# Kernel optimization log

Measured on AMD Instinct MI355X. Metric: run time of the kernel, lower is better.

Reference implementation:

```python
import jax, jax.numpy as jnp
import numpy as np

NEG_SLOPE = 0.2  # PyG GATConv default negative_slope
H, C = 4, 64     # heads, per-head channels


def gat_layer(x, src, dst, edge_attr, W, a_src, a_dst, We, a_e, b):
    """PyG-style GATConv with edge features, concat=True. src/dst include self loops."""
    N = x.shape[0]
    h = (x @ W).reshape(N, H, C)                      # [N,H,C]
    al_s = (h * a_src[None]).sum(-1)                  # [N,H]
    al_d = (h * a_dst[None]).sum(-1)                  # [N,H]
    eh = (edge_attr @ We).reshape(-1, H, C)           # [E,H,C]
    al_e = (eh * a_e[None]).sum(-1)                   # [E,H]
    alpha = jax.nn.leaky_relu(al_s[src] + al_d[dst] + al_e, NEG_SLOPE)  # [E,H]
    # softmax over incoming edges of each destination node
    m = jax.ops.segment_max(alpha, dst, num_segments=N)
    p = jnp.exp(alpha - m[dst])
    denom = jax.ops.segment_sum(p, dst, num_segments=N)
    w = p / (denom[dst] + 1e-16)                      # [E,H]
    msg = h[src] * w[..., None]                       # [E,H,C]
    out = jax.ops.segment_sum(msg, dst, num_segments=N)  # [N,H,C]
    return out.reshape(N, H * C) + b


def setup_inputs() -> dict:
    key = jax.random.key(0)
    ks = jax.random.split(key, 20)
    N, E = 50000, 800000
    s = 0.05
    inp = {
        'x': jax.random.normal(ks[0], (N, 5), jnp.float32),
        'edge_index': jax.random.randint(ks[1], (2, E), 0, N, jnp.int32),
        'edge_attr': jax.random.normal(ks[2], (E, 4), jnp.float32),
        'W0': jax.random.normal(ks[3], (5, 256), jnp.float32) * s,
        'a_src0': jax.random.normal(ks[4], (H, C), jnp.float32) * s,
        'a_dst0': jax.random.normal(ks[5], (H, C), jnp.float32) * s,
        'We0': jax.random.normal(ks[6], (4, 256), jnp.float32) * s,
        'a_e0': jax.random.normal(ks[7], (H, C), jnp.float32) * s,
        'b0': jnp.zeros((256,), jnp.float32),
        'W1': jax.random.normal(ks[8], (256, 256), jnp.float32) * s,
        'a_src1': jax.random.normal(ks[9], (H, C), jnp.float32) * s,
        'a_dst1': jax.random.normal(ks[10], (H, C), jnp.float32) * s,
        'We1': jax.random.normal(ks[11], (4, 256), jnp.float32) * s,
        'a_e1': jax.random.normal(ks[12], (H, C), jnp.float32) * s,
        'b1': jnp.zeros((256,), jnp.float32),
        'Wm1': jax.random.normal(ks[13], (768, 128), jnp.float32) * s,
        'bm1': jnp.zeros((128,), jnp.float32),
        'Wm2': jax.random.normal(ks[14], (128, 64), jnp.float32) * s,
        'bm2': jnp.zeros((64,), jnp.float32),
        'Wm3': jax.random.normal(ks[15], (64, 128), jnp.float32) * s,
        'bm3': jnp.zeros((128,), jnp.float32),
    }
    return inp


def reference(x, edge_index, edge_attr,
              W0, a_src0, a_dst0, We0, a_e0, b0,
              W1, a_src1, a_dst1, We1, a_e1, b1,
              Wm1, bm1, Wm2, bm2, Wm3, bm3):
    N = x.shape[0]
    # add self loops once; self-loop edge_attr = mean of edge_attr (PyG fill_value='mean')
    loops = jnp.arange(N, dtype=edge_index.dtype)
    src = jnp.concatenate([edge_index[0], loops])
    dst = jnp.concatenate([edge_index[1], loops])
    mean_ea = jnp.mean(edge_attr, axis=0, keepdims=True)
    ea = jnp.concatenate([edge_attr, jnp.broadcast_to(mean_ea, (N, edge_attr.shape[1]))], axis=0)

    h = gat_layer(x, src, dst, ea, W0, a_src0, a_dst0, We0, a_e0, b0)
    h = jax.nn.relu(h)  # dropout is identity in eval
    h = gat_layer(h, src, dst, ea, W1, a_src1, a_dst1, We1, a_e1, b1)

    mean_pool = jnp.mean(h, axis=0)                      # [256]
    max_pool = jnp.max(h, axis=0)                        # [256]
    att = jax.nn.softmax(jnp.sum(h * mean_pool[None], axis=1))  # [N]
    att_pool = jnp.sum(h * att[:, None], axis=0)         # [256]
    comb = jnp.concatenate([mean_pool, max_pool, att_pool])  # [768]

    z = jax.nn.relu(comb @ Wm1 + bm1)
    z = jax.nn.relu(z @ Wm2 + bm2)
    g = z @ Wm3 + bm3
    return g[None]  # [1,128]
```

## Files before the change

### kernel.cpp

```cpp
#include <hip/hip_runtime.h>
#include <hip/hip_fp16.h>
#include <type_traits>

static const long long N_ = 50000;
static const long long E_ = 800000;
static const int NCOPY = 8;
#define LOG2E 1.44269504088896f

typedef __attribute__((ext_vector_type(8))) short bf16x8;
typedef __attribute__((ext_vector_type(4))) float f32x4;

__device__ __forceinline__ float lrelu(float x){ return x >= 0.f ? x : 0.2f*x; }
__device__ __forceinline__ unsigned fkey(float x){
  unsigned u = __float_as_uint(x);
  return (u & 0x80000000u) ? ~u : (u | 0x80000000u);
}
__device__ __forceinline__ float unfkey(unsigned k){
  return __uint_as_float((k & 0x80000000u) ? (k & 0x7fffffffu) : ~k);
}
__device__ __forceinline__ unsigned h2u(__half2 h){ return *(unsigned*)&h; }

__global__ void k_pre(const int* __restrict__ ei, int* __restrict__ deg8,
                      unsigned char* __restrict__ rank,
                      const float* __restrict__ W1, ushort* __restrict__ Bhi,
                      ushort* __restrict__ Blo){
  int t = threadIdx.x;
  long long e = (long long)blockIdx.x*256 + t;
  if (e < E_){
    int d = ei[E_ + e];
    int copy = blockIdx.x & (NCOPY-1);
    int old = atomicAdd(&deg8[copy*(int)N_ + d], 1);
    rank[e] = (unsigned char)old;
  }
  if (blockIdx.x < 256){
    int k = blockIdx.x, n = t;
    float v = W1[k*256+n];
    unsigned u = __float_as_uint(v);
    ushort hi = (ushort)(u>>16);
    float rem = v - __uint_as_float(u & 0xffff0000u);
    unsigned ur = __float_as_uint(rem);
    ushort lo = (ushort)((ur + 0x7fff + ((ur>>16)&1)) >> 16);
    int tl = n>>4, kb = k>>5, q = (k>>3)&3, j = k&7;
    long long idx = ((((long long)tl*8+kb)*64 + q*16 + (n&15))<<3) + j;
    Bhi[idx] = hi; Blo[idx] = lo;
  }
}

__global__ void k_scan1(const int* __restrict__ deg8, int* __restrict__ bsum,
                        const float* __restrict__ ea, float* __restrict__ eapart){
  __shared__ int lds[256];
  __shared__ float fl[256];
  int t = threadIdx.x;
  long long idx = (long long)blockIdx.x*256 + t;
  int v = 0;
  if (idx < N_){
    #pragma unroll
    for (int c=0;c<NCOPY;c++) v += deg8[c*(int)N_ + idx];
  }
  lds[t] = v;
  float s = 0.f;
  for (long long i = (long long)blockIdx.x*256 + t; i < E_*4; i += (long long)gridDim.x*256)
    s += ea[i];
  fl[t] = s;
  __syncthreads();
  for (int st=128; st>=1; st>>=1){
    if (t<st) lds[t] += lds[t+st];
    if (t<st && st>=4) fl[t] += fl[t+st];
    __syncthreads();
  }
  if (t==0) bsum[blockIdx.x] = lds[0];
  if (t<4) eapart[blockIdx.x*4 + t] = fl[t];
}

__global__ void k_scan2(const int* __restrict__ bsum, int* __restrict__ bpre, int nb,
                        int* __restrict__ rowptr,
                        const float* __restrict__ We0, const float* __restrict__ ae0,
                        const float* __restrict__ We1, const float* __restrict__ ae1,
                        const float* __restrict__ eapart, float* __restrict__ small){
  __shared__ int lds[256];
  __shared__ float sea[4];
  int t = threadIdx.x;
  int v = (t < nb) ? bsum[t] : 0;
  lds[t] = v; __syncthreads();
  for (int off=1; off<256; off<<=1){
    int add = (t>=off) ? lds[t-off] : 0;
    __syncthreads();
    lds[t] += add;
    __syncthreads();
  }
  if (t < nb) bpre[t] = lds[t] - v;
  if (t == 0) rowptr[N_] = (int)E_;
  if (t < 4){
    float s = 0.f;
    for (int b=0;b<nb;b++) s += eapart[b*4+t];
    sea[t] = s;
  }
  if (t < 32){
    int l = t>>4, f = (t>>2)&3, h = t&3;
    const float* We = l ? We1 : We0;
    const float* ae = l ? ae1 : ae0;
    float s = 0.f;
    for (int cc=0; cc<64; cc++) s += We[f*256 + h*64 + cc]*ae[h*64+cc];
    small[l*16 + f*4 + h] = s * LOG2E;
  }
  __syncthreads();
  if (t < 8){
    int l = t>>2, h = t&3;
    const float* Ae = small + l*16;
    const float invE = 1.f/(float)E_;
    float s = 0.f;
    for (int f=0; f<4; f++) s += sea[f]*invE*Ae[f*4+h];
    small[32 + l*4 + h] = s;
  }
}

__global__ void k_scan3(const int* __restrict__ deg8, const int* __restrict__ bpre,
                        int* __restrict__ rowptr, int* __restrict__ base){
  __shared__ int lds[256];
  int t = threadIdx.x;
  long long idx = (long long)blockIdx.x*256 + t;
  int dd[NCOPY]; int v = 0;
  if (idx < N_){
    #pragma unroll
    for (int c=0;c<NCOPY;c++){ dd[c] = deg8[c*(int)N_ + idx]; v += dd[c]; }
  }
  lds[t] = v; __syncthreads();
  for (int off=1; off<256; off<<=1){
    int add = (t>=off) ? lds[t-off] : 0;
    __syncthreads();
    lds[t] += add;
    __syncthreads();
  }
  if (idx < N_){
    int rp = bpre[blockIdx.x] + lds[t] - v;
    rowptr[idx] = rp;
    int cum = rp;
    #pragma unroll
    for (int c=0;c<NCOPY;c++){ base[c*(int)N_ + idx] = cum; cum += dd[c]; }
  }
}

__global__ void k_h0(const float* __restrict__ x, const float* __restrict__ W0,
                     const float* __restrict__ as0, const float* __restrict__ ad0,
                     __half* __restrict__ h0, float* __restrict__ als, float* __restrict__ ald){
  int wid = (int)(((long long)blockIdx.x*blockDim.x + threadIdx.x) >> 6);
  int lane = threadIdx.x & 63;
  if (wid >= (int)N_) return;
  const float* xr = x + wid*5;
  float xv[5];
  #pragma unroll
  for (int f=0; f<5; f++) xv[f] = xr[f];
  int c = lane*4;
  float a0=0,a1=0,a2=0,a3=0;
  #pragma unroll
  for (int f=0; f<5; f++){
    const float* wr = W0 + f*256 + c;
    a0 += xv[f]*wr[0]; a1 += xv[f]*wr[1]; a2 += xv[f]*wr[2]; a3 += xv[f]*wr[3];
  }
  uint2 pk = make_uint2(h2u(__floats2half2_rn(a0,a1)), h2u(__floats2half2_rn(a2,a3)));
  *(uint2*)(h0 + wid*256 + c) = pk;
  const float* asp = as0 + c;
  const float* adp = ad0 + c;
  float ss = a0*asp[0]+a1*asp[1]+a2*asp[2]+a3*asp[3];
  float dd = a0*adp[0]+a1*adp[1]+a2*adp[2]+a3*adp[3];
  int head = lane>>4;
  #pragma unroll
  for (int m=1; m<16; m<<=1){ ss += __shfl_xor(ss, m); dd += __shfl_xor(dd, m); }
  if ((lane&15)==0){ als[wid*4+head]=ss*LOG2E; ald[wid*4+head]=dd*LOG2E; }
}

__global__ void k_scatter(const int* __restrict__ ei, const float* __restrict__ ea,
                          const int* __restrict__ base, const unsigned char* __restrict__ rank,
                          int2* __restrict__ csr2, uint4* __restrict__ pe,
                          const float* __restrict__ small,
                          const float* __restrict__ als0, const float* __restrict__ ald0){
  long long e = (long long)blockIdx.x*256 + threadIdx.x;
  if (e >= E_) return;
  int s = ei[e], d = ei[E_+e];
  int copy = blockIdx.x & (NCOPY-1);
  int pos = base[copy*(int)N_ + d] + (int)rank[e];
  csr2[pos] = make_int2(s, d);
  float4 v = *(const float4*)(ea + e*4);
  float4 As = *(const float4*)(als0 + s*4);
  float4 Ad = *(const float4*)(ald0 + d*4);
  float as_[4] = {As.x,As.y,As.z,As.w};
  float ad_[4] = {Ad.x,Ad.y,Ad.z,Ad.w};
  float p0[4], o1[4];
  #pragma unroll
  for (int h=0; h<4; h++){
    float a0 = v.x*small[0+h]  + v.y*small[4+h]  + v.z*small[8+h]  + v.w*small[12+h];
    p0[h] = exp2f(lrelu(as_[h] + ad_[h] + a0));
    o1[h] = v.x*small[16+h] + v.y*small[20+h] + v.z*small[24+h] + v.w*small[28+h];
  }
  uint4 pk = make_uint4(h2u(__floats2half2_rn(p0[0],p0[1])),
                        h2u(__floats2half2_rn(p0[2],p0[3])),
                        h2u(__floats2half2_rn(o1[0],o1[1])),
                        h2u(__floats2half2_rn(o1[2],o1[3])));
  pe[pos] = pk;
}

__global__ void k_palpha1(const int2* __restrict__ csr2, const uint4* __restrict__ pe,
                          const float* __restrict__ als1, const float* __restrict__ ald1,
                          __half* __restrict__ p1h){
  long long i = (long long)blockIdx.x*256 + threadIdx.x;
  if (i >= E_) return;
  int2 sd = csr2[i];
  float4 As = *(const float4*)(als1 + sd.x*4);
  float4 Ad = *(const float4*)(ald1 + sd.y*4);
  uint4 pk = pe[i];
  float2 e01 = __half22float2(*(__half2*)&pk.z);
  float2 e23 = __half22float2(*(__half2*)&pk.w);
  float p0 = exp2f(lrelu(As.x+Ad.x+e01.x));
  float p1 = exp2f(lrelu(As.y+Ad.y+e01.y));
  float p2 = exp2f(lrelu(As.z+Ad.z+e23.x));
  float p3 = exp2f(lrelu(As.w+Ad.w+e23.y));
  uint2 o = make_uint2(h2u(__floats2half2_rn(p0,p1)), h2u(__floats2half2_rn(p2,p3)));
  *(uint2*)(p1h + i*4) = o;
}

template<typename OutT, bool RELU>
__global__ __launch_bounds__(256) void k_agg(const __half* __restrict__ hin,
    const float* __restrict__ als, const float* __restrict__ ald,
    const int* __restrict__ rowptr, const int2* __restrict__ csr2,
    const __half* __restrict__ ph, int pstride,
    const float* __restrict__ small, int loop_off,
    const float* __restrict__ bias, OutT* __restrict__ out){
  int wid = (int)(((long long)blockIdx.x*256 + threadIdx.x) >> 6);
  int lane = threadIdx.x & 63;
  if (wid >= (int)N_) return;
  int half_ = lane>>5, l5 = lane&31;
  int head = l5>>3, c8 = l5*8;
  const uint4* hp = (const uint4*)hin;
  float a[8]; float den;
  {
    float pS = exp2f(lrelu(als[wid*4+head] + ald[wid*4+head] + small[loop_off+head]));
    float pp = (half_==0) ? pS : 0.f;
    uint4 r = hp[wid*32 + l5];
    float2 f0 = __half22float2(*(__half2*)&r.x);
    float2 f1 = __half22float2(*(__half2*)&r.y);
    float2 f2 = __half22float2(*(__half2*)&r.z);
    float2 f3 = __half22float2(*(__half2*)&r.w);
    den = pp;
    a[0]=pp*f0.x; a[1]=pp*f0.y; a[2]=pp*f1.x; a[3]=pp*f1.y;
    a[4]=pp*f2.x; a[5]=pp*f2.y; a[6]=pp*f3.x; a[7]=pp*f3.y;
  }
  int beg = rowptr[wid], end = rowptr[wid+1];
  int i = beg;
  for (; i+7 < end; i += 8){
    int   sv[4]; float pv[4]; uint4 rr[4];
    #pragma unroll
    for (int k=0;k<4;k++){
      int e = i + 2*k + half_;
      sv[k] = csr2[e].x;
      pv[k] = __half2float(ph[e*pstride + head]);
    }
    #pragma unroll
    for (int k=0;k<4;k++) rr[k] = hp[sv[k]*32 + l5];
    #pragma unroll
    for (int k=0;k<4;k++){
      float2 f0 = __half22float2(*(__half2*)&rr[k].x);
      float2 f1 = __half22float2(*(__half2*)&rr[k].y);
      float2 f2 = __half22float2(*(__half2*)&rr[k].z);
      float2 f3 = __half22float2(*(__half2*)&rr[k].w);
      float p = pv[k];
      den += p;
      a[0]+=p*f0.x; a[1]+=p*f0.y; a[2]+=p*f1.x; a[3]+=p*f1.y;
      a[4]+=p*f2.x; a[5]+=p*f2.y; a[6]+=p*f3.x; a[7]+=p*f3.y;
    }
  }
  for (; i < end; i += 2){
    int e = i + half_;
    bool act = (e < end);
    int ee = act ? e : (end-1);
    int s0 = csr2[ee].x;
    float p = act ? __half2float(ph[ee*pstride + head]) : 0.f;
    uint4 r = hp[s0*32 + l5];
    float2 f0 = __half22float2(*(__half2*)&r.x);
    float2 f1 = __half22float2(*(__half2*)&r.y);
    float2 f2 = __half22float2(*(__half2*)&r.z);
    float2 f3 = __half22float2(*(__half2*)&r.w);
    den += p;
    a[0]+=p*f0.x; a[1]+=p*f0.y; a[2]+=p*f1.x; a[3]+=p*f1.y;
    a[4]+=p*f2.x; a[5]+=p*f2.y; a[6]+=p*f3.x; a[7]+=p*f3.y;
  }
  den += __shfl_xor(den, 32);
  #pragma unroll
  for (int j=0;j<8;j++) a[j] += __shfl_xor(a[j], 32);
  if (half_ == 0){
    float inv = 1.f/(den + 1e-16f);
    float4 b0 = *(const float4*)(bias + c8);
    float4 b1 = *(const float4*)(bias + c8 + 4);
    float o[8];
    o[0]=a[0]*inv+b0.x; o[1]=a[1]*inv+b0.y; o[2]=a[2]*inv+b0.z; o[3]=a[3]*inv+b0.w;
    o[4]=a[4]*inv+b1.x; o[5]=a[5]*inv+b1.y; o[6]=a[6]*inv+b1.z; o[7]=a[7]*inv+b1.w;
    if (RELU){
      #pragma unroll
      for (int j=0;j<8;j++) o[j] = fmaxf(o[j], 0.f);
    }
    if constexpr (std::is_same<OutT,__half>::value){
      uint4 qk = make_uint4(h2u(__floats2half2_rn(o[0],o[1])), h2u(__floats2half2_rn(o[2],o[3])),
                            h2u(__floats2half2_rn(o[4],o[5])), h2u(__floats2half2_rn(o[6],o[7])));
      *(uint4*)(out + wid*256 + c8) = qk;
    } else {
      *(float4*)(out + wid*256 + c8)     = make_float4(o[0],o[1],o[2],o[3]);
      *(float4*)(out + wid*256 + c8 + 4) = make_float4(o[4],o[5],o[6],o[7]);
    }
  }
}

__global__ __launch_bounds__(256) void k_gemm(const float* __restrict__ A,
    const ushort* __restrict__ Bhi, const ushort* __restrict__ Blo,
    __half* __restrict__ Ch, const float* __restrict__ as1, const float* __restrict__ ad1,
    float* __restrict__ als, float* __restrict__ ald){
  __shared__ ushort Ah[32*264];
  __shared__ ushort Al[32*264];
  int t = threadIdx.x;
  long long base = (long long)blockIdx.x*32;
  for (int i=t; i<2048; i+=256){
    int r = i>>6, q4 = i&63;
    float4 v = make_float4(0.f,0.f,0.f,0.f);
    if (base + r < N_) v = *(const float4*)(A + (base+r)*256 + q4*4);
    float vv[4] = {v.x,v.y,v.z,v.w};
    ushort hh[4], ll[4];
    #pragma unroll
    for (int e=0;e<4;e++){
      unsigned u = __float_as_uint(vv[e]);
      hh[e] = (ushort)(u>>16);
      float rem = vv[e] - __uint_as_float(u & 0xffff0000u);
      unsigned ur = __float_as_uint(rem);
      ll[e] = (ushort)((ur + 0x7fff + ((ur>>16)&1)) >> 16);
    }
    int off = r*264 + q4*4;
    *(ushort4*)(Ah+off) = make_ushort4(hh[0],hh[1],hh[2],hh[3]);
    *(ushort4*)(Al+off) = make_ushort4(ll[0],ll[1],ll[2],ll[3]);
  }
  __syncthreads();
  int w = t>>6, lane = t&63, m = lane&15, q = lane>>4;
  int rbase = (w>>1)*16;
  int nhalf = (w&1)*8;
  f32x4 acc[8];
  #pragma unroll
  for (int i=0;i<8;i++) acc[i] = (f32x4){0.f,0.f,0.f,0.f};
  for (int kb=0; kb<8; kb++){
    int aoff = (rbase+m)*264 + kb*32 + q*8;
    bf16x8 ah = *(const bf16x8*)(Ah + aoff);
    bf16x8 al = *(const bf16x8*)(Al + aoff);
    #pragma unroll
    for (int tt=0; tt<8; tt++){
      long long bidx = ((((long long)(nhalf+tt)*8+kb)*64 + lane)<<3);
      bf16x8 bh = *(const bf16x8*)(Bhi + bidx);
      bf16x8 bl = *(const bf16x8*)(Blo + bidx);
      acc[tt] = __builtin_amdgcn_mfma_f32_16x16x32_bf16(ah, bh, acc[tt], 0,0,0);
      acc[tt] = __builtin_amdgcn_mfma_f32_16x16x32_bf16(al, bh, acc[tt], 0,0,0);
      acc[tt] = __builtin_amdgcn_mfma_f32_16x16x32_bf16(ah, bl, acc[tt], 0,0,0);
    }
  }
  float ssv[4][2], ddv[4][2];
  #pragma unroll
  for (int r=0;r<4;r++){ ssv[r][0]=0.f; ssv[r][1]=0.f; ddv[r][0]=0.f; ddv[r][1]=0.f; }
  #pragma unroll
  for (int tt=0; tt<8; tt++){
    int col = (nhalf+tt)*16 + m;
    float as_ = as1[col], ad_ = ad1[col];
    int hh = tt>>2;
    #pragma unroll
    for (int r=0;r<4;r++){
      ssv[r][hh] += acc[tt][r]*as_;
      ddv[r][hh] += acc[tt][r]*ad_;
    }
  }
  #pragma unroll
  for (int r=0;r<4;r++){
    #pragma unroll
    for (int hh=0; hh<2; hh++){
      #pragma unroll
      for (int mm=1; mm<16; mm<<=1){
        ssv[r][hh] += __shfl_xor(ssv[r][hh], mm);
        ddv[r][hh] += __shfl_xor(ddv[r][hh], mm);
      }
    }
  }
  #pragma unroll
  for (int r=0;r<4;r++){
    long long grow = base + rbase + q*4 + r;
    if (grow < N_){
      #pragma unroll
      for (int tt=0; tt<8; tt++)
        Ch[grow*256 + (nhalf+tt)*16 + m] = __float2half(acc[tt][r]);
      if (m==0){
        int hb = (w&1)*2;
        als[grow*4 + hb+0] = ssv[r][0]*LOG2E;
        ald[grow*4 + hb+0] = ddv[r][0]*LOG2E;
        als[grow*4 + hb+1] = ssv[r][1]*LOG2E;
        ald[grow*4 + hb+1] = ddv[r][1]*LOG2E;
      }
    }
  }
}

__global__ void k_pool1(const __half* __restrict__ h2, float* __restrict__ sum_pool,
                        unsigned* __restrict__ maxkey){
  int c = threadIdx.x;
  float s = 0.f; float m = -3.4e38f;
  for (long long n = blockIdx.x; n < N_; n += gridDim.x){
    float v = __half2float(h2[n*256+c]); s += v; m = fmaxf(m, v);
  }
  atomicAdd(&sum_pool[c], s);
  atomicMax(&maxkey[c], fkey(m));
}

__global__ void k_atts(const __half* __restrict__ h2, const float* __restrict__ sum_pool,
                       float* __restrict__ ssum, float* __restrict__ att_raw){
  __shared__ float part[4][256];
  __shared__ float es[4];
  int t = threadIdx.x; int lane = t&63; int w = t>>6;
  const float invN = 1.f/(float)N_;
  int c = lane*4;
  float4 mp = *(const float4*)(sum_pool + c);
  float esum = 0.f;
  float acc0=0.f, acc1=0.f, acc2=0.f, acc3=0.f;
  for (long long wid = (long long)blockIdx.x*4 + w; wid < N_; wid += (long long)gridDim.x*4){
    uint2 pk = *(const uint2*)(h2 + wid*256 + c);
    float2 a01 = __half22float2(*(__half2*)&pk.x);
    float2 a23 = __half22float2(*(__half2*)&pk.y);
    float s = (a01.x*mp.x + a01.y*mp.y + a23.x*mp.z + a23.y*mp.w)*invN;
    #pragma unroll
    for (int m=1; m<64; m<<=1) s += __shfl_xor(s, m);
    float e = __expf(s);
    if (lane==0) esum += e;
    acc0 += e*a01.x; acc1 += e*a01.y; acc2 += e*a23.x; acc3 += e*a23.y;
  }
  part[w][c+0]=acc0; part[w][c+1]=acc1; part[w][c+2]=acc2; part[w][c+3]=acc3;
  if (lane==0) es[w] = esum;
  __syncthreads();
  if (t < 256){
    float v = part[0][t]+part[1][t]+part[2][t]+part[3][t];
    atomicAdd(&att_raw[t], v);
  }
  if (t==0) atomicAdd(ssum, es[0]+es[1]+es[2]+es[3]);
}

__global__ void k_mlp(const float* __restrict__ sum_pool, const unsigned* __restrict__ maxkey,
                      const float* __restrict__ att_raw, const float* __restrict__ ssum,
                      const float* __restrict__ Wm1, const float* __restrict__ bm1,
                      const float* __restrict__ Wm2, const float* __restrict__ bm2,
                      const float* __restrict__ Wm3, const float* __restrict__ bm3,
                      float* __restrict__ out){
  __shared__ float comb[768];
  __shared__ float z1p[4][128]; __shared__ float z1[128];
  __shared__ float z2p[8][64];  __shared__ float z2[64];
  __shared__ float z3p[4][128];
  int t = threadIdx.x;
  const float invN = 1.f/(float)N_;
  float invS = 1.f/(*ssum);
  for (int i=t; i<768; i+=512){
    float v;
    if (i < 256)      v = sum_pool[i]*invN;
    else if (i < 512) v = unfkey(maxkey[i-256]);
    else              v = att_raw[i-512]*invS;
    comb[i] = v;
  }
  __syncthreads();
  { int n = t&127, part = t>>7;
    float a = 0.f;
    for (int f=part*192; f<part*192+192; f++) a += comb[f]*Wm1[f*128+n];
    z1p[part][n] = a;
  }
  __syncthreads();
  if (t < 128)
    z1[t] = fmaxf(bm1[t] + z1p[0][t]+z1p[1][t]+z1p[2][t]+z1p[3][t], 0.f);
  __syncthreads();
  { int n = t&63, part = t>>6;
    float a = 0.f;
    for (int f=part*16; f<part*16+16; f++) a += z1[f]*Wm2[f*64+n];
    z2p[part][n] = a;
  }
  __syncthreads();
  if (t < 64){
    float a = bm2[t];
    #pragma unroll
    for (int p=0;p<8;p++) a += z2p[p][t];
    z2[t] = fmaxf(a, 0.f);
  }
  __syncthreads();
  { int n = t&127, part = t>>7;
    float a = 0.f;
    for (int f=part*16; f<part*16+16; f++) a += z2[f]*Wm3[f*128+n];
    z3p[part][n] = a;
  }
  __syncthreads();
  if (t < 128)
    out[t] = bm3[t] + z3p[0][t]+z3p[1][t]+z3p[2][t]+z3p[3][t];
}

extern "C" void kernel_launch(void* const* d_in, const int* in_sizes, int n_in,
                              void* d_out, int out_size, void* d_ws, size_t ws_size,
                              hipStream_t stream){
  (void)in_sizes; (void)n_in; (void)out_size; (void)ws_size;
  const float* x   = (const float*)d_in[0];
  const int*   ei  = (const int*)d_in[1];
  const float* ea  = (const float*)d_in[2];
  const float* W0  = (const float*)d_in[3];
  const float* as0 = (const float*)d_in[4];
  const float* ad0 = (const float*)d_in[5];
  const float* We0 = (const float*)d_in[6];
  const float* ae0 = (const float*)d_in[7];
  const float* b0  = (const float*)d_in[8];
  const float* W1  = (const float*)d_in[9];
  const float* as1 = (const float*)d_in[10];
  const float* ad1 = (const float*)d_in[11];
  const float* We1 = (const float*)d_in[12];
  const float* ae1 = (const float*)d_in[13];
  const float* b1  = (const float*)d_in[14];
  const float* Wm1 = (const float*)d_in[15];
  const float* bm1 = (const float*)d_in[16];
  const float* Wm2 = (const float*)d_in[17];
  const float* bm2 = (const float*)d_in[18];
  const float* Wm3 = (const float*)d_in[19];
  const float* bm3 = (const float*)d_in[20];
  float* out = (float*)d_out;

  char* ws = (char*)d_ws;
  size_t o = 0;
  auto alloc = [&](size_t bytes)->size_t{
    size_t r = o; o = (o + bytes + 255) & ~(size_t)255; return r;
  };
  size_t o_bufF   = alloc((size_t)N_*256*4);
  size_t o_bufH   = alloc((size_t)N_*256*2);
  size_t o_als0   = alloc((size_t)N_*4*4);
  size_t o_ald0   = alloc((size_t)N_*4*4);
  size_t o_als1   = alloc((size_t)N_*4*4);
  size_t o_ald1   = alloc((size_t)N_*4*4);
  size_t o_rowptr = alloc((size_t)(N_+1)*4);
  size_t o_csr2   = alloc((size_t)E_*8);
  size_t o_pe     = alloc((size_t)E_*16);
  size_t o_p1     = alloc((size_t)E_*4*2);
  size_t o_rank   = alloc((size_t)E_);
  size_t o_base   = alloc((size_t)NCOPY*N_*4);
  size_t o_Bhi    = alloc((size_t)256*256*2);
  size_t o_Blo    = alloc((size_t)256*256*2);
  size_t o_bsum   = alloc(256*4);
  size_t o_bpre   = alloc(256*4);
  size_t o_eapart = alloc(256*4*4);
  size_t zstart   = o;
  size_t o_deg8   = alloc((size_t)NCOPY*N_*4);
  size_t o_sumpool= alloc(256*4);
  size_t o_maxkey = alloc(256*4);
  size_t o_attraw = alloc(256*4);
  size_t o_ssum   = alloc(4);
  size_t zend     = o;
  size_t o_small  = alloc(40*4);

  float*  bufF   = (float*)(ws + o_bufF);
  __half* bufH   = (__half*)(ws + o_bufH);
  __half* h2h    = (__half*)(ws + o_bufF);
  float* pals0  = (float*)(ws + o_als0);
  float* pald0  = (float*)(ws + o_ald0);
  float* pals1  = (float*)(ws + o_als1);
  float* pald1  = (float*)(ws + o_ald1);
  int*   rowptr = (int*)(ws + o_rowptr);
  int2*  csr2   = (int2*)(ws + o_csr2);
  uint4* pe     = (uint4*)(ws + o_pe);
  __half* p1h   = (__half*)(ws + o_p1);
  unsigned char* rank = (unsigned char*)(ws + o_rank);
  int*   base   = (int*)(ws + o_base);
  ushort* Bhi   = (ushort*)(ws + o_Bhi);
  ushort* Blo   = (ushort*)(ws + o_Blo);
  int*   bsum   = (int*)(ws + o_bsum);
  int*   bpre   = (int*)(ws + o_bpre);
  float* eapart = (float*)(ws + o_eapart);
  int*   deg8   = (int*)(ws + o_deg8);
  float* sumpool= (float*)(ws + o_sumpool);
  unsigned* maxkey = (unsigned*)(ws + o_maxkey);
  float* attraw = (float*)(ws + o_attraw);
  float* ssum   = (float*)(ws + o_ssum);
  float* small  = (float*)(ws + o_small);

  hipMemsetAsync(ws + zstart, 0, zend - zstart, stream);

  int eb = (int)((E_ + 255)/256);
  int nb_wave = (int)((N_*64 + 255)/256);
  int gb = (int)((N_ + 31)/32);
  int sb = (int)((N_ + 255)/256);

  k_pre    <<<eb, 256, 0, stream>>>(ei, deg8, rank, W1, Bhi, Blo);
  k_scan1  <<<sb, 256, 0, stream>>>(deg8, bsum, ea, eapart);
  k_scan2  <<<1, 256, 0, stream>>>(bsum, bpre, sb, rowptr,
                                   We0, ae0, We1, ae1, eapart, small);
  k_scan3  <<<sb, 256, 0, stream>>>(deg8, bpre, rowptr, base);
  k_h0     <<<nb_wave, 256, 0, stream>>>(x, W0, as0, ad0, bufH, pals0, pald0);
  k_scatter<<<eb, 256, 0, stream>>>(ei, ea, base, rank, csr2, pe,
                                    small, pals0, pald0);
  k_agg<float,true>  <<<nb_wave, 256, 0, stream>>>(bufH, pals0, pald0, rowptr, csr2,
                                         (const __half*)pe, 8, small, 32, b0, bufF);
  k_gemm   <<<gb, 256, 0, stream>>>(bufF, Bhi, Blo, bufH, as1, ad1, pals1, pald1);
  k_palpha1<<<eb, 256, 0, stream>>>(csr2, pe, pals1, pald1, p1h);
  k_agg<__half,false><<<nb_wave, 256, 0, stream>>>(bufH, pals1, pald1, rowptr, csr2,
                                         p1h, 4, small, 36, b1, h2h);
  k_pool1  <<<256, 256, 0, stream>>>(h2h, sumpool, maxkey);
  k_atts   <<<256, 256, 0, stream>>>(h2h, sumpool, ssum, attraw);
  k_mlp    <<<1, 512, 0, stream>>>(sumpool, maxkey, attraw, ssum,
                                   Wm1, bm1, Wm2, bm2, Wm3, bm3, out);
}
```

Measured before the change: 494.9 us.

## Fuse h0 into k_pre, inline layer-1 attention into aggregation, shrink CSR

Folds the layer-0 projection kernel into the degree-counting pre-pass, so each block also handles 16 nodes. Removes the separate layer-1 alpha kernel and instead computes exp2(lrelu(als+ald+ae)) inside the second aggregation, reading the edge term from pe at an offset. It stores only source indices in the CSR (int instead of int2), which halves index traffic. The aggregation unroll goes from 4 to 6 edge pairs for more memory-level parallelism. The trade-off is an extra gather of als per edge and more register pressure in the aggregation kernel.

Measured after the change: 494.0 us. No clear change (-0.2%).

```diff
diff --git a/kernel.cpp b/kernel.cpp
--- a/kernel.cpp
+++ b/kernel.cpp
@@ -23,7 +23,11 @@
 __global__ void k_pre(const int* __restrict__ ei, int* __restrict__ deg8,
                       unsigned char* __restrict__ rank,
                       const float* __restrict__ W1, ushort* __restrict__ Bhi,
-                      ushort* __restrict__ Blo){
+                      ushort* __restrict__ Blo,
+                      const float* __restrict__ x, const float* __restrict__ W0,
+                      const float* __restrict__ as0, const float* __restrict__ ad0,
+                      __half* __restrict__ h0, float* __restrict__ als,
+                      float* __restrict__ ald){
   int t = threadIdx.x;
   long long e = (long long)blockIdx.x*256 + t;
   if (e < E_){
@@ -43,6 +47,32 @@
     int tl = n>>4, kb = k>>5, q = (k>>3)&3, j = k&7;
     long long idx = ((((long long)tl*8+kb)*64 + q*16 + (n&15))<<3) + j;
     Bhi[idx] = hi; Blo[idx] = lo;
+  }
+  int w = t>>6, lane = t&63;
+  int c = lane*4, head = lane>>4;
+  #pragma unroll
+  for (int rep=0; rep<4; rep++){
+    int wid = blockIdx.x*16 + w*4 + rep;
+    if (wid >= (int)N_) break;
+    const float* xr = x + wid*5;
+    float xv[5];
+    #pragma unroll
+    for (int f=0; f<5; f++) xv[f] = xr[f];
+    float a0=0,a1=0,a2=0,a3=0;
+    #pragma unroll
+    for (int f=0; f<5; f++){
+      const float* wr = W0 + f*256 + c;
+      a0 += xv[f]*wr[0]; a1 += xv[f]*wr[1]; a2 += xv[f]*wr[2]; a3 += xv[f]*wr[3];
+    }
+    uint2 pk = make_uint2(h2u(__floats2half2_rn(a0,a1)), h2u(__floats2half2_rn(a2,a3)));
+    *(uint2*)(h0 + (long long)wid*256 + c) = pk;
+    const float* asp = as0 + c;
+    const float* adp = ad0 + c;
+    float ss = a0*asp[0]+a1*asp[1]+a2*asp[2]+a3*asp[3];
+    float dd = a0*adp[0]+a1*adp[1]+a2*adp[2]+a3*adp[3];
+    #pragma unroll
+    for (int m=1; m<16; m<<=1){ ss += __shfl_xor(ss, m); dd += __shfl_xor(dd, m); }
+    if ((lane&15)==0){ als[wid*4+head]=ss*LOG2E; ald[wid*4+head]=dd*LOG2E; }
   }
 }
 
@@ -140,38 +170,9 @@
   }
 }
 
-__global__ void k_h0(const float* __restrict__ x, const float* __restrict__ W0,
-                     const float* __restrict__ as0, const float* __restrict__ ad0,
-                     __half* __restrict__ h0, float* __restrict__ als, float* __restrict__ ald){
-  int wid = (int)(((long long)blockIdx.x*blockDim.x + threadIdx.x) >> 6);
-  int lane = threadIdx.x & 63;
-  if (wid >= (int)N_) return;
-  const float* xr = x + wid*5;
-  float xv[5];
-  #pragma unroll
-  for (int f=0; f<5; f++) xv[f] = xr[f];
-  int c = lane*4;
-  float a0=0,a1=0,a2=0,a3=0;
-  #pragma unroll
-  for (int f=0; f<5; f++){
-    const float* wr = W0 + f*256 + c;
-    a0 += xv[f]*wr[0]; a1 += xv[f]*wr[1]; a2 += xv[f]*wr[2]; a3 += xv[f]*wr[3];
-  }
-  uint2 pk = make_uint2(h2u(__floats2half2_rn(a0,a1)), h2u(__floats2half2_rn(a2,a3)));
-  *(uint2*)(h0 + wid*256 + c) = pk;
-  const float* asp = as0 + c;
-  const float* adp = ad0 + c;
-  float ss = a0*asp[0]+a1*asp[1]+a2*asp[2]+a3*asp[3];
-  float dd = a0*adp[0]+a1*adp[1]+a2*adp[2]+a3*adp[3];
-  int head = lane>>4;
-  #pragma unroll
-  for (int m=1; m<16; m<<=1){ ss += __shfl_xor(ss, m); dd += __shfl_xor(dd, m); }
-  if ((lane&15)==0){ als[wid*4+head]=ss*LOG2E; ald[wid*4+head]=dd*LOG2E; }
-}
-
 __global__ void k_scatter(const int* __restrict__ ei, const float* __restrict__ ea,
                           const int* __restrict__ base, const unsigned char* __restrict__ rank,
-                          int2* __restrict__ csr2, uint4* __restrict__ pe,
+                          int* __restrict__ csrs, uint4* __restrict__ pe,
                           const float* __restrict__ small,
                           const float* __restrict__ als0, const float* __restrict__ ald0){
   long long e = (long long)blockIdx.x*256 + threadIdx.x;
@@ -179,7 +180,7 @@
   int s = ei[e], d = ei[E_+e];
   int copy = blockIdx.x & (NCOPY-1);
   int pos = base[copy*(int)N_ + d] + (int)rank[e];
-  csr2[pos] = make_int2(s, d);
+  csrs[pos] = s;
   float4 v = *(const float4*)(ea + e*4);
   float4 As = *(const float4*)(als0 + s*4);
   float4 Ad = *(const float4*)(ald0 + d*4);
@@ -199,30 +200,11 @@
   pe[pos] = pk;
 }
 
-__global__ void k_palpha1(const int2* __restrict__ csr2, const uint4* __restrict__ pe,
-                          const float* __restrict__ als1, const float* __restrict__ ald1,
-                          __half* __restrict__ p1h){
-  long long i = (long long)blockIdx.x*256 + threadIdx.x;
-  if (i >= E_) return;
-  int2 sd = csr2[i];
-  float4 As = *(const float4*)(als1 + sd.x*4);
-  float4 Ad = *(const float4*)(ald1 + sd.y*4);
-  uint4 pk = pe[i];
-  float2 e01 = __half22float2(*(__half2*)&pk.z);
-  float2 e23 = __half22float2(*(__half2*)&pk.w);
-  float p0 = exp2f(lrelu(As.x+Ad.x+e01.x));
-  float p1 = exp2f(lrelu(As.y+Ad.y+e01.y));
-  float p2 = exp2f(lrelu(As.z+Ad.z+e23.x));
-  float p3 = exp2f(lrelu(As.w+Ad.w+e23.y));
-  uint2 o = make_uint2(h2u(__floats2half2_rn(p0,p1)), h2u(__floats2half2_rn(p2,p3)));
-  *(uint2*)(p1h + i*4) = o;
-}
-
-template<typename OutT, bool RELU>
+template<typename OutT, bool RELU, bool INLINE_P>
 __global__ __launch_bounds__(256) void k_agg(const __half* __restrict__ hin,
     const float* __restrict__ als, const float* __restrict__ ald,
-    const int* __restrict__ rowptr, const int2* __restrict__ csr2,
-    const __half* __restrict__ ph, int pstride,
+    const int* __restrict__ rowptr, const int* __restrict__ csrs,
+    const __half* __restrict__ ph, int pstride, int poff,
     const float* __restrict__ small, int loop_off,
     const float* __restrict__ bias, OutT* __restrict__ out){
   int wid = (int)(((long long)blockIdx.x*256 + threadIdx.x) >> 6);
@@ -231,9 +213,10 @@
   int half_ = lane>>5, l5 = lane&31;
   int head = l5>>3, c8 = l5*8;
   const uint4* hp = (const uint4*)hin;
+  float aldv = ald[wid*4+head];
   float a[8]; float den;
   {
-    float pS = exp2f(lrelu(als[wid*4+head] + ald[wid*4+head] + small[loop_off+head]));
+    float pS = exp2f(lrelu(als[wid*4+head] + aldv + small[loop_off+head]));
     float pp = (half_==0) ? pS : 0.f;
     uint4 r = hp[wid*32 + l5];
     float2 f0 = __half22float2(*(__half2*)&r.x);
@@ -246,18 +229,26 @@
   }
   int beg = rowptr[wid], end = rowptr[wid+1];
   int i = beg;
-  for (; i+7 < end; i += 8){
-    int   sv[4]; float pv[4]; uint4 rr[4];
-    #pragma unroll
-    for (int k=0;k<4;k++){
+  const int UN = 6;
+  for (; i + 2*UN-1 < end; i += 2*UN){
+    int sv[UN]; float pv[UN]; uint4 rr[UN];
+    #pragma unroll
+    for (int k=0;k<UN;k++) sv[k] = csrs[i + 2*k + half_];
+    #pragma unroll
+    for (int k=0;k<UN;k++) rr[k] = hp[sv[k]*32 + l5];
+    #pragma unroll
+    for (int k=0;k<UN;k++){
       int e = i + 2*k + half_;
-      sv[k] = csr2[e].x;
-      pv[k] = __half2float(ph[e*pstride + head]);
-    }
-    #pragma unroll
-    for (int k=0;k<4;k++) rr[k] = hp[sv[k]*32 + l5];
-    #pragma unroll
-    for (int k=0;k<4;k++){
+      if (INLINE_P){
+        float alev = __half2float(ph[e*pstride + poff + head]);
+        float alsv = als[sv[k]*4 + head];
+        pv[k] = exp2f(lrelu(alsv + aldv + alev));
+      } else {
+        pv[k] = __half2float(ph[e*pstride + poff + head]);
+      }
+    }
+    #pragma unroll
+    for (int k=0;k<UN;k++){
       float2 f0 = __half22float2(*(__half2*)&rr[k].x);
       float2 f1 = __half22float2(*(__half2*)&rr[k].y);
       float2 f2 = __half22float2(*(__half2*)&rr[k].z);
@@ -272,8 +263,16 @@
     int e = i + half_;
     bool act = (e < end);
     int ee = act ? e : (end-1);
-    int s0 = csr2[ee].x;
-    float p = act ? __half2float(ph[ee*pstride + head]) : 0.f;
+    int s0 = csrs[ee];
+    float p;
+    if (INLINE_P){
+      float alev = __half2float(ph[ee*pstride + poff + head]);
+      float alsv = als[s0*4 + head];
+      p = exp2f(lrelu(alsv + aldv + alev));
+    } else {
+      p = __half2float(ph[ee*pstride + poff + head]);
+    }
+    if (!act) p = 0.f;
     uint4 r = hp[s0*32 + l5];
     float2 f0 = __half22float2(*(__half2*)&r.x);
     float2 f1 = __half22float2(*(__half2*)&r.y);
@@ -300,10 +299,10 @@
     if constexpr (std::is_same<OutT,__half>::value){
       uint4 qk = make_uint4(h2u(__floats2half2_rn(o[0],o[1])), h2u(__floats2half2_rn(o[2],o[3])),
                             h2u(__floats2half2_rn(o[4],o[5])), h2u(__floats2half2_rn(o[6],o[7])));
-      *(uint4*)(out + wid*256 + c8) = qk;
+      *(uint4*)(out + (long long)wid*256 + c8) = qk;
     } else {
-      *(float4*)(out + wid*256 + c8)     = make_float4(o[0],o[1],o[2],o[3]);
-      *(float4*)(out + wid*256 + c8 + 4) = make_float4(o[4],o[5],o[6],o[7]);
+      *(float4*)(out + (long long)wid*256 + c8)     = make_float4(o[0],o[1],o[2],o[3]);
+      *(float4*)(out + (long long)wid*256 + c8 + 4) = make_float4(o[4],o[5],o[6],o[7]);
     }
   }
 }
@@ -532,9 +531,8 @@
   size_t o_als1   = alloc((size_t)N_*4*4);
   size_t o_ald1   = alloc((size_t)N_*4*4);
   size_t o_rowptr = alloc((size_t)(N_+1)*4);
-  size_t o_csr2   = alloc((size_t)E_*8);
+  size_t o_csrs   = alloc((size_t)E_*4);
   size_t o_pe     = alloc((size_t)E_*16);
-  size_t o_p1     = alloc((size_t)E_*4*2);
   size_t o_rank   = alloc((size_t)E_);
   size_t o_base   = alloc((size_t)NCOPY*N_*4);
   size_t o_Bhi    = alloc((size_t)256*256*2);
@@ -559,9 +557,8 @@
   float* pals1  = (float*)(ws + o_als1);
   float* pald1  = (float*)(ws + o_ald1);
   int*   rowptr = (int*)(ws + o_rowptr);
-  int2*  csr2   = (int2*)(ws + o_csr2);
+  int*   csrs   = (int*)(ws + o_csrs);
   uint4* pe     = (uint4*)(ws + o_pe);
-  __half* p1h   = (__half*)(ws + o_p1);
   unsigned char* rank = (unsigned char*)(ws + o_rank);
   int*   base   = (int*)(ws + o_base);
   ushort* Bhi   = (ushort*)(ws + o_Bhi);
@@ -583,20 +580,19 @@
   int gb = (int)((N_ + 31)/32);
   int sb = (int)((N_ + 255)/256);
 
-  k_pre    <<<eb, 256, 0, stream>>>(ei, deg8, rank, W1, Bhi, Blo);
+  k_pre    <<<eb, 256, 0, stream>>>(ei, deg8, rank, W1, Bhi, Blo,
+                                    x, W0, as0, ad0, bufH, pals0, pald0);
   k_scan1  <<<sb, 256, 0, stream>>>(deg8, bsum, ea, eapart);
   k_scan2  <<<1, 256, 0, stream>>>(bsum, bpre, sb, rowptr,
                                    We0, ae0, We1, ae1, eapart, small);
   k_scan3  <<<sb, 256, 0, stream>>>(deg8, bpre, rowptr, base);
-  k_h0     <<<nb_wave, 256, 0, stream>>>(x, W0, as0, ad0, bufH, pals0, pald0);
-  k_scatter<<<eb, 256, 0, stream>>>(ei, ea, base, rank, csr2, pe,
+  k_scatter<<<eb, 256, 0, stream>>>(ei, ea, base, rank, csrs, pe,
                                     small, pals0, pald0);
-  k_agg<float,true>  <<<nb_wave, 256, 0, stream>>>(bufH, pals0, pald0, rowptr, csr2,
-                                         (const __half*)pe, 8, small, 32, b0, bufF);
+  k_agg<float,true,false> <<<nb_wave, 256, 0, stream>>>(bufH, pals0, pald0, rowptr, csrs,
+                                         (const __half*)pe, 8, 0, small, 32, b0, bufF);
   k_gemm   <<<gb, 256, 0, stream>>>(bufF, Bhi, Blo, bufH, as1, ad1, pals1, pald1);
-  k_palpha1<<<eb, 256, 0, stream>>>(csr2, pe, pals1, pald1, p1h);
-  k_agg<__half,false><<<nb_wave, 256, 0, stream>>>(bufH, pals1, pald1, rowptr, csr2,
-                                         p1h, 4, small, 36, b1, h2h);
+  k_agg<__half,false,true><<<nb_wave, 256, 0, stream>>>(bufH, pals1, pald1, rowptr, csrs,
+                                         (const __half*)pe, 8, 4, small, 36, b1, h2h);
   k_pool1  <<<256, 256, 0, stream>>>(h2h, sumpool, maxkey);
   k_atts   <<<256, 256, 0, stream>>>(h2h, sumpool, ssum, attraw);
   k_mlp    <<<1, 512, 0, stream>>>(sumpool, maxkey, attraw, ssum,
```
